# Optimization experiments

Hardware: AMD Instinct MI355X
Metric: run time of the kernel (lower is better)

## Reference

```python
import jax, jax.numpy as jnp
import numpy as np

# ---- static radial-binning geometry for a 64x64 grid (classic azimuthalAverage) ----
_N = 64
_yy, _xx = np.indices((_N, _N))
_cx = (_xx.max() - _xx.min()) / 2.0  # 31.5
_cy = (_yy.max() - _yy.min()) / 2.0  # 31.5
_r = np.hypot(_xx - _cx, _yy - _cy)
_rint = _r.astype(int).ravel()                 # (4096,) integer radius per pixel
_NBINS = int(_rint.max()) + 1                  # 45 distinct integer radii (0..44)
_counts = np.bincount(_rint, minlength=_NBINS).astype(np.float32)
# classic azimuthalAverage (cumsum-of-sorted trick) returns bins 1 .. NBINS-2 inclusive
_ONEHOT = jnp.asarray(np.eye(_NBINS, dtype=np.float32)[_rint])  # (4096, 45) scatter matrix
_NR = jnp.asarray(_counts[1:_NBINS - 1])       # (43,) pixels per returned bin


def _tke(x):
    # x: (B, T, 2, 64, 64) -> turbulent kinetic energy (B, 64, 64)
    x = x.reshape(x.shape[0], -1, 2, _N, _N)
    mean_flow = jnp.mean(x, axis=1, keepdims=True)
    tur = jnp.mean((x - mean_flow) ** 2, axis=1)   # (B, 2, 64, 64) per-component variance
    return (tur[:, 0] + tur[:, 1]) * 0.5


def _spectrum(x):
    # TKE -> 2D power spectrum -> radial (azimuthal) average, all batched.
    tke = _tke(x)
    sp = jnp.fft.fftshift(jnp.fft.fft2(tke), axes=(-2, -1))
    power = jnp.real(sp * jnp.conj(sp)).reshape(x.shape[0], -1)  # (B, 4096)
    sums = power @ _ONEHOT                          # (B, 45) per-integer-radius sums
    return sums[:, 1:_NBINS - 1] / _NR              # (B, 43) azimuthal average


def setup_inputs() -> dict:
    key = jax.random.key(0)
    k1, k2 = jax.random.split(key)
    preds = jax.random.normal(k1, (64, 60, 2, 64, 64), dtype=jnp.float32)
    trues = jax.random.normal(k2, (64, 60, 2, 64, 64), dtype=jnp.float32)
    return {"preds": preds, "trues": trues}


def reference(preds, trues):
    # SpectrumLoss with loss = MSE: loss(tke2spectrum(trues), tke2spectrum(preds))
    sp_t = _spectrum(trues)
    sp_p = _spectrum(preds)
    return jnp.mean((sp_t - sp_p) ** 2)
```

## Files before the change

### kernel.cpp

```cpp
#include <hip/hip_runtime.h>
#include <math.h>

#define TT 60
#define BB 64
#define STR 68
#define NBINS 45

__global__ __launch_bounds__(256, 4) void tke_kernel(const float* __restrict__ preds,
                                                     const float* __restrict__ trues,
                                                     float* __restrict__ tke) {
    int gtid  = blockIdx.x * 256 + threadIdx.x;
    int input = gtid >> 16;
    int rem   = gtid & 65535;
    int b     = rem >> 10;
    int p4    = rem & 1023;

    const float4* src  = (const float4*)(input ? trues : preds);
    const float4* base = src + (size_t)b * (TT * 2048) + p4;

    float su[4]  = {0, 0, 0, 0}, squ[4] = {0, 0, 0, 0};
    float sv[4]  = {0, 0, 0, 0}, sqv[4] = {0, 0, 0, 0};

    #pragma unroll
    for (int tb = 0; tb < TT; tb += 5) {
        float4 r[10];
        #pragma unroll
        for (int i = 0; i < 5; ++i) {
            r[2 * i]     = base[(tb + i) * 2048];
            r[2 * i + 1] = base[(tb + i) * 2048 + 1024];
        }
        __builtin_amdgcn_sched_barrier(0);
        #pragma unroll
        for (int i = 0; i < 5; ++i) {
            float4 u = r[2 * i], v = r[2 * i + 1];
            su[0] += u.x; squ[0] += u.x * u.x; sv[0] += v.x; sqv[0] += v.x * v.x;
            su[1] += u.y; squ[1] += u.y * u.y; sv[1] += v.y; sqv[1] += v.y * v.y;
            su[2] += u.z; squ[2] += u.z * u.z; sv[2] += v.z; sqv[2] += v.z * v.z;
            su[3] += u.w; squ[3] += u.w * u.w; sv[3] += v.w; sqv[3] += v.w * v.w;
        }
    }

    const float inv = 1.0f / 60.0f;
    float o[4];
    #pragma unroll
    for (int j = 0; j < 4; ++j) {
        float mu = su[j] * inv, mv = sv[j] * inv;
        o[j] = 0.5f * ((squ[j] * inv - mu * mu) + (sqv[j] * inv - mv * mv));
    }
    float4 outv; outv.x = o[0]; outv.y = o[1]; outv.z = o[2]; outv.w = o[3];
    ((float4*)tke)[(size_t)(input * BB + b) * 1024 + p4] = outv;
}

__global__ __launch_bounds__(512) void dft_kernel(const float* __restrict__ tke,
                                                  float* __restrict__ binsums) {
    __shared__ __align__(16) float tke_s[64 * 64];
    __shared__ __align__(16) float Gr[64 * STR];
    __shared__ __align__(16) float Gi[64 * STR];
    __shared__ float ctab[64], stab[64];
    __shared__ float bins_s[NBINS];

    int tid = threadIdx.x;
    int img = blockIdx.x;

    if (tid < 64) {
        float ang = (float)tid * 0.09817477042468103871f;
        float ss, cc;
        sincosf(ang, &ss, &cc);
        ctab[tid] = cc; stab[tid] = ss;
    }
    if (tid < NBINS) bins_s[tid] = 0.0f;

    {
        const float4* src = (const float4*)(tke + (size_t)img * 4096);
        float4* dst = (float4*)tke_s;
        for (int i = tid; i < 1024; i += 512) dst[i] = src[i];
    }
    __syncthreads();

    {
        int k  = tid >> 3;
        int x0 = (tid & 7) * 8;
        float gr[8] = {0,0,0,0,0,0,0,0};
        float gi[8] = {0,0,0,0,0,0,0,0};
        for (int y = 0; y < 64; ++y) {
            float4 ta = *(const float4*)&tke_s[(y << 6) + x0];
            float4 tb = *(const float4*)&tke_s[(y << 6) + x0 + 4];
            float tv[8] = {ta.x, ta.y, ta.z, ta.w, tb.x, tb.y, tb.z, tb.w};
            int idx = (k * y) & 63;
            float cc = ctab[idx], ss = stab[idx];
            #pragma unroll
            for (int j = 0; j < 8; ++j) {
                gr[j] += cc * tv[j];
                gi[j] -= ss * tv[j];
            }
        }
        #pragma unroll
        for (int j = 0; j < 8; ++j) {
            Gr[(x0 + j) * STR + k] = gr[j];
            Gi[(x0 + j) * STR + k] = gi[j];
        }
    }
    __syncthreads();

    {
        int l  = tid >> 3;
        int k0 = (tid & 7) * 8;
        float fr[8] = {0,0,0,0,0,0,0,0};
        float fi[8] = {0,0,0,0,0,0,0,0};
        for (int x = 0; x < 64; ++x) {
            float4 a0 = *(const float4*)&Gr[x * STR + k0];
            float4 a1 = *(const float4*)&Gr[x * STR + k0 + 4];
            float4 b0 = *(const float4*)&Gi[x * STR + k0];
            float4 b1 = *(const float4*)&Gi[x * STR + k0 + 4];
            float ar[8] = {a0.x, a0.y, a0.z, a0.w, a1.x, a1.y, a1.z, a1.w};
            float br[8] = {b0.x, b0.y, b0.z, b0.w, b1.x, b1.y, b1.z, b1.w};
            int idx = (l * x) & 63;
            float cc = ctab[idx], ss = stab[idx];
            #pragma unroll
            for (int j = 0; j < 8; ++j) {
                fr[j] += ar[j] * cc + br[j] * ss;
                fi[j] += br[j] * cc - ar[j] * ss;
            }
        }
        float fl = (float)((l + 32) & 63) - 31.5f;
        #pragma unroll
        for (int j = 0; j < 8; ++j) {
            int k = k0 + j;
            float fk = (float)((k + 32) & 63) - 31.5f;
            float r = sqrtf(fk * fk + fl * fl);
            int bin = (int)r;
            float pw = fr[j] * fr[j] + fi[j] * fi[j];
            atomicAdd(&bins_s[bin], pw);
        }
    }
    __syncthreads();
    if (tid < NBINS) binsums[img * NBINS + tid] = bins_s[tid];
}

__global__ __launch_bounds__(256) void loss_kernel(const float* __restrict__ binsums,
                                                   float* __restrict__ out) {
    __shared__ int   cnt[NBINS];
    __shared__ float part[256];
    int tid = threadIdx.x;
    if (tid < NBINS) cnt[tid] = 0;
    __syncthreads();
    for (int p = tid; p < 4096; p += 256) {
        float dy = (float)(p >> 6) - 31.5f;
        float dx = (float)(p & 63) - 31.5f;
        int bin = (int)sqrtf(dy * dy + dx * dx);
        atomicAdd(&cnt[bin], 1);
    }
    __syncthreads();
    float acc = 0.0f;
    for (int j = tid; j < BB * 43; j += 256) {
        int b   = j / 43;
        int bin = j - b * 43 + 1;
        float n  = (float)cnt[bin];
        float st = binsums[(BB + b) * NBINS + bin] / n;
        float sp = binsums[b * NBINS + bin] / n;
        float d  = st - sp;
        acc += d * d;
    }
    part[tid] = acc;
    __syncthreads();
    for (int s = 128; s > 0; s >>= 1) {
        if (tid < s) part[tid] += part[tid + s];
        __syncthreads();
    }
    if (tid == 0) out[0] = part[0] * (1.0f / (BB * 43.0f));
}

extern "C" void kernel_launch(void* const* d_in, const int* in_sizes, int n_in,
                              void* d_out, int out_size, void* d_ws, size_t ws_size,
                              hipStream_t stream) {
    const float* preds = (const float*)d_in[0];
    const float* trues = (const float*)d_in[1];
    float* tke     = (float*)d_ws;
    float* binsums = tke + 2 * BB * 4096;

    tke_kernel<<<512, 256, 0, stream>>>(preds, trues, tke);
    dft_kernel<<<128, 512, 0, stream>>>(tke, binsums);
    loss_kernel<<<1, 256, 0, stream>>>(binsums, (float*)d_out);
}
```

Measured before the change: 73.10 us.

## Split TKE time reduction across four waves with shared-memory combine

The TKE kernel now assigns 64 pixel-quads per block and splits the 60 time steps into four chunks of 15, one per wavefront, and combines the partial sums through shared memory. Four times as many blocks are launched, raising memory-level parallelism for this bandwidth-bound streaming reduction, whose old grid had only 512 blocks. The cost is an LDS round trip and a barrier per block, plus three of four waves sitting idle during the final variance computation.

```diff
diff --git a/kernel.cpp b/kernel.cpp
--- a/kernel.cpp
+++ b/kernel.cpp
@@ -6,23 +6,30 @@
 #define STR 68
 #define NBINS 45
 
-__global__ __launch_bounds__(256, 4) void tke_kernel(const float* __restrict__ preds,
+__global__ __launch_bounds__(256, 6) void tke_kernel(const float* __restrict__ preds,
                                                      const float* __restrict__ trues,
                                                      float* __restrict__ tke) {
-    int gtid  = blockIdx.x * 256 + threadIdx.x;
-    int input = gtid >> 16;
-    int rem   = gtid & 65535;
-    int b     = rem >> 10;
-    int p4    = rem & 1023;
+    __shared__ float4 red[3][256];
+
+    int tid = threadIdx.x;
+    int p   = tid & 63;
+    int tc  = tid >> 6;
+
+    int bid   = blockIdx.x;
+    int input = bid >> 10;
+    int rem   = bid & 1023;
+    int b     = rem >> 4;
+    int pg    = rem & 15;
+    int p4    = pg * 64 + p;
 
     const float4* src  = (const float4*)(input ? trues : preds);
-    const float4* base = src + (size_t)b * (TT * 2048) + p4;
-
-    float su[4]  = {0, 0, 0, 0}, squ[4] = {0, 0, 0, 0};
-    float sv[4]  = {0, 0, 0, 0}, sqv[4] = {0, 0, 0, 0};
+    const float4* base = src + (size_t)b * (TT * 2048) + (size_t)(tc * 15) * 2048 + p4;
+
+    float4 su  = {0, 0, 0, 0}, squ = {0, 0, 0, 0};
+    float4 sv  = {0, 0, 0, 0}, sqv = {0, 0, 0, 0};
 
     #pragma unroll
-    for (int tb = 0; tb < TT; tb += 5) {
+    for (int tb = 0; tb < 15; tb += 5) {
         float4 r[10];
         #pragma unroll
         for (int i = 0; i < 5; ++i) {
@@ -33,22 +40,45 @@
         #pragma unroll
         for (int i = 0; i < 5; ++i) {
             float4 u = r[2 * i], v = r[2 * i + 1];
-            su[0] += u.x; squ[0] += u.x * u.x; sv[0] += v.x; sqv[0] += v.x * v.x;
-            su[1] += u.y; squ[1] += u.y * u.y; sv[1] += v.y; sqv[1] += v.y * v.y;
-            su[2] += u.z; squ[2] += u.z * u.z; sv[2] += v.z; sqv[2] += v.z * v.z;
-            su[3] += u.w; squ[3] += u.w * u.w; sv[3] += v.w; sqv[3] += v.w * v.w;
-        }
-    }
-
-    const float inv = 1.0f / 60.0f;
-    float o[4];
-    #pragma unroll
-    for (int j = 0; j < 4; ++j) {
-        float mu = su[j] * inv, mv = sv[j] * inv;
-        o[j] = 0.5f * ((squ[j] * inv - mu * mu) + (sqv[j] * inv - mv * mv));
-    }
-    float4 outv; outv.x = o[0]; outv.y = o[1]; outv.z = o[2]; outv.w = o[3];
-    ((float4*)tke)[(size_t)(input * BB + b) * 1024 + p4] = outv;
+            su.x += u.x; squ.x += u.x * u.x; sv.x += v.x; sqv.x += v.x * v.x;
+            su.y += u.y; squ.y += u.y * u.y; sv.y += v.y; sqv.y += v.y * v.y;
+            su.z += u.z; squ.z += u.z * u.z; sv.z += v.z; sqv.z += v.z * v.z;
+            su.w += u.w; squ.w += u.w * u.w; sv.w += v.w; sqv.w += v.w * v.w;
+        }
+    }
+
+    if (tc != 0) {
+        red[tc - 1][0 * 64 + p] = su;
+        red[tc - 1][1 * 64 + p] = squ;
+        red[tc - 1][2 * 64 + p] = sv;
+        red[tc - 1][3 * 64 + p] = sqv;
+    }
+    __syncthreads();
+
+    if (tc == 0) {
+        #pragma unroll
+        for (int s = 0; s < 3; ++s) {
+            float4 a = red[s][0 * 64 + p], c = red[s][1 * 64 + p];
+            float4 d = red[s][2 * 64 + p], e = red[s][3 * 64 + p];
+            su.x += a.x; su.y += a.y; su.z += a.z; su.w += a.w;
+            squ.x += c.x; squ.y += c.y; squ.z += c.z; squ.w += c.w;
+            sv.x += d.x; sv.y += d.y; sv.z += d.z; sv.w += d.w;
+            sqv.x += e.x; sqv.y += e.y; sqv.z += e.z; sqv.w += e.w;
+        }
+        const float inv = 1.0f / 60.0f;
+        float4 o;
+        {
+            float mu = su.x * inv, mv = sv.x * inv;
+            o.x = 0.5f * ((squ.x * inv - mu * mu) + (sqv.x * inv - mv * mv));
+            mu = su.y * inv; mv = sv.y * inv;
+            o.y = 0.5f * ((squ.y * inv - mu * mu) + (sqv.y * inv - mv * mv));
+            mu = su.z * inv; mv = sv.z * inv;
+            o.z = 0.5f * ((squ.z * inv - mu * mu) + (sqv.z * inv - mv * mv));
+            mu = su.w * inv; mv = sv.w * inv;
+            o.w = 0.5f * ((squ.w * inv - mu * mu) + (sqv.w * inv - mv * mv));
+        }
+        ((float4*)tke)[(size_t)(input * BB + b) * 1024 + p4] = o;
+    }
 }
 
 __global__ __launch_bounds__(512) void dft_kernel(const float* __restrict__ tke,
@@ -178,7 +208,7 @@
     float* tke     = (float*)d_ws;
     float* binsums = tke + 2 * BB * 4096;
 
-    tke_kernel<<<512, 256, 0, stream>>>(preds, trues, tke);
+    tke_kernel<<<2048, 256, 0, stream>>>(preds, trues, tke);
     dft_kernel<<<128, 512, 0, stream>>>(tke, binsums);
     loss_kernel<<<1, 256, 0, stream>>>(binsums, (float*)d_out);
 }
```

After: 71.72 us. No clear change (-1.9%).
